# Optimization experiments

Measured on AMD Instinct MI355X. Metric: run time of the kernel, lower is better.

Reference implementation:

```python
import jax, jax.numpy as jnp
import numpy as np

H_BINS = 64
SIGMA = 0.02
EPS = 1e-6


def setup_inputs() -> dict:
    key = jax.random.key(0)
    x = jax.random.uniform(key, (8, 3, 256, 256), dtype=jnp.float32)
    return {"x": x}


def reference(x):
    h = H_BINS
    L = x.shape[0]
    x = jnp.clip(x, 0.0, 1.0)
    I = x.reshape(L, 3, -1)                      # [L,3,N]
    Iy = jnp.sqrt(jnp.sum(I * I, axis=1) + EPS)  # [L,N] pixel intensity
    logs = jnp.log(I + EPS)                      # [L,3,N]
    # per-channel log-chromaticity: for c=0:(u=l0-l1, v=l0-l2); c=1:(l1-l0, l1-l2); c=2:(l2-l0, l2-l1)
    cu = jnp.array([1, 0, 0])
    cv = jnp.array([2, 2, 1])
    U = logs - logs[:, cu, :]                    # [L,3,N]
    V = logs - logs[:, cv, :]                    # [L,3,N]
    offset = jnp.linspace(-3.0, 3.0, h, dtype=jnp.float32)  # [h]
    inv_s2 = jnp.float32(1.0 / (SIGMA * SIGMA))
    # RBF-like (inverse-quadratic) soft binning kernels: [L,3,N,h]
    Ku = 1.0 / (1.0 + jnp.square(U[..., None] - offset) * inv_s2)
    Kv = 1.0 / (1.0 + jnp.square(V[..., None] - offset) * inv_s2)
    # weighted outer-product reduction over pixels -> [L,3,h,h]
    hists = jnp.einsum('ln,lcnu,lcnv->lcuv', Iy, Ku, Kv)
    # normalize each sample by its total mass
    total = jnp.sum(hists, axis=(1, 2, 3), keepdims=True)
    return hists / (total + EPS)
```

## Files before the change

### kernel.cpp

```cpp
#include <hip/hip_runtime.h>

#define H 64
#define NPIX 65536
#define LBATCH 8
#define LC 24
#define S_CHUNKS 32
#define PB 2048
#define EPSF 1e-6f
#define LN2_50 34.6573590f

typedef _Float16 h8 __attribute__((ext_vector_type(8)));
typedef __fp16   g2 __attribute__((ext_vector_type(2)));
typedef float f32x16 __attribute__((ext_vector_type(16)));
union H8u { h8 v8; g2 v2[4]; };

#define KEV(d) __builtin_amdgcn_rcpf(fmaf((d), (d), 1.0f))
#define PK(a, b) __builtin_amdgcn_cvt_pkrtz((a), (b))

__global__ __launch_bounds__(256) void hist_zero(float* __restrict__ out) {
    out[blockIdx.x * 256 + threadIdx.x] = 0.0f;
}

__global__ __launch_bounds__(256, 3) void hist_main(const float* __restrict__ x,
                                                    float* __restrict__ out) {
    __shared__ float sU[PB];
    __shared__ float sV[PB];
    __shared__ float sW[PB];
    __shared__ float sHist[H * H];

    const int tid  = threadIdx.x;
    const int wv   = tid >> 6;
    const int lane = tid & 63;
    const int hf   = lane >> 5;
    const int ln   = lane & 31;
    const int lc   = blockIdx.y;
    const int l    = lc / 3;
    const int c    = lc - 3 * l;

    #pragma unroll
    for (int r = 0; r < 4; r++)
        *(float4*)&sHist[(r * 256 + tid) * 4] = make_float4(0.f, 0.f, 0.f, 0.f);

    const float* __restrict__ x0p = x + (l * 3 + 0) * NPIX;
    const float* __restrict__ x1p = x + (l * 3 + 1) * NPIX;
    const float* __restrict__ x2p = x + (l * 3 + 2) * NPIX;
    const int base = blockIdx.x * PB;

    #pragma unroll
    for (int pass = 0; pass < 2; pass++) {
        const int ploc = pass * 1024 + tid * 4;
        const float4 r0 = *(const float4*)&x0p[base + ploc];
        const float4 r1 = *(const float4*)&x1p[base + ploc];
        const float4 r2 = *(const float4*)&x2p[base + ploc];
        float4 U4, V4, W4;
        #define PREP(E) { \
            const float v0 = fminf(fmaxf(r0.E, 0.0f), 1.0f); \
            const float v1 = fminf(fmaxf(r1.E, 0.0f), 1.0f); \
            const float v2 = fminf(fmaxf(r2.E, 0.0f), 1.0f); \
            W4.E = __builtin_amdgcn_sqrtf(fmaf(v0, v0, fmaf(v1, v1, fmaf(v2, v2, EPSF)))); \
            const float lg0 = __builtin_amdgcn_logf(v0 + EPSF); \
            const float lg1 = __builtin_amdgcn_logf(v1 + EPSF); \
            const float lg2 = __builtin_amdgcn_logf(v2 + EPSF); \
            float U, V; \
            if (c == 0)      { U = lg0 - lg1; V = lg0 - lg2; } \
            else if (c == 1) { U = lg1 - lg0; V = lg1 - lg2; } \
            else             { U = lg2 - lg0; V = lg2 - lg1; } \
            U4.E = LN2_50 * U; V4.E = LN2_50 * V; }
        PREP(x) PREP(y) PREP(z) PREP(w)
        #undef PREP
        *(float4*)&sU[ploc] = U4;
        *(float4*)&sV[ploc] = V4;
        *(float4*)&sW[ploc] = W4;
    }
    __syncthreads();

    const float step50 = 50.0f * (6.0f / 63.0f);
    const float ou0 = -150.0f + step50 * (float)ln;
    const float ou1 = ou0 + step50 * 32.0f;

    f32x16 acc00, acc01, acc10, acc11;
    #pragma unroll
    for (int i = 0; i < 16; i++) { acc00[i] = 0.f; acc01[i] = 0.f; acc10[i] = 0.f; acc11[i] = 0.f; }

    const int wbase = wv * 512;
    #pragma unroll 2
    for (int ks = 0; ks < 32; ks++) {
        const int kb = wbase + ks * 16 + hf * 8;
        const float4 ua = *(const float4*)&sU[kb];
        const float4 ub = *(const float4*)&sU[kb + 4];
        const float4 va = *(const float4*)&sV[kb];
        const float4 vb = *(const float4*)&sV[kb + 4];
        const float4 wa = *(const float4*)&sW[kb];
        const float4 wb = *(const float4*)&sW[kb + 4];
        H8u A0, A1, B0, B1;
        A0.v2[0] = PK(wa.x * KEV(ua.x - ou0), wa.y * KEV(ua.y - ou0));
        A0.v2[1] = PK(wa.z * KEV(ua.z - ou0), wa.w * KEV(ua.w - ou0));
        A0.v2[2] = PK(wb.x * KEV(ub.x - ou0), wb.y * KEV(ub.y - ou0));
        A0.v2[3] = PK(wb.z * KEV(ub.z - ou0), wb.w * KEV(ub.w - ou0));
        A1.v2[0] = PK(wa.x * KEV(ua.x - ou1), wa.y * KEV(ua.y - ou1));
        A1.v2[1] = PK(wa.z * KEV(ua.z - ou1), wa.w * KEV(ua.w - ou1));
        A1.v2[2] = PK(wb.x * KEV(ub.x - ou1), wb.y * KEV(ub.y - ou1));
        A1.v2[3] = PK(wb.z * KEV(ub.z - ou1), wb.w * KEV(ub.w - ou1));
        B0.v2[0] = PK(KEV(va.x - ou0), KEV(va.y - ou0));
        B0.v2[1] = PK(KEV(va.z - ou0), KEV(va.w - ou0));
        B0.v2[2] = PK(KEV(vb.x - ou0), KEV(vb.y - ou0));
        B0.v2[3] = PK(KEV(vb.z - ou0), KEV(vb.w - ou0));
        B1.v2[0] = PK(KEV(va.x - ou1), KEV(va.y - ou1));
        B1.v2[1] = PK(KEV(va.z - ou1), KEV(va.w - ou1));
        B1.v2[2] = PK(KEV(vb.x - ou1), KEV(vb.y - ou1));
        B1.v2[3] = PK(KEV(vb.z - ou1), KEV(vb.w - ou1));
        acc00 = __builtin_amdgcn_mfma_f32_32x32x16_f16(A0.v8, B0.v8, acc00, 0, 0, 0);
        acc01 = __builtin_amdgcn_mfma_f32_32x32x16_f16(A0.v8, B1.v8, acc01, 0, 0, 0);
        acc10 = __builtin_amdgcn_mfma_f32_32x32x16_f16(A1.v8, B0.v8, acc10, 0, 0, 0);
        acc11 = __builtin_amdgcn_mfma_f32_32x32x16_f16(A1.v8, B1.v8, acc11, 0, 0, 0);
    }

    #pragma unroll
    for (int r = 0; r < 16; r++) {
        const int row = (r & 3) + 8 * (r >> 2) + 4 * hf;
        atomicAdd(&sHist[row * 64 + ln],             acc00[r]);
        atomicAdd(&sHist[row * 64 + 32 + ln],        acc01[r]);
        atomicAdd(&sHist[(row + 32) * 64 + ln],      acc10[r]);
        atomicAdd(&sHist[(row + 32) * 64 + 32 + ln], acc11[r]);
    }
    __syncthreads();

    float* __restrict__ g = out + lc * (H * H);
    #pragma unroll
    for (int r = 0; r < 16; r++) {
        const int i = r * 256 + tid;
        unsafeAtomicAdd(&g[i], sHist[i]);
    }
}

__global__ __launch_bounds__(256) void hist_finish(float* __restrict__ out) {
    const int l = blockIdx.x;
    float* __restrict__ p = out + l * 3 * H * H;
    float s = 0.0f;
    #pragma unroll
    for (int it = 0; it < 12; it++) {
        const float4 v = *(const float4*)&p[(it * 256 + threadIdx.x) * 4];
        s += (v.x + v.y) + (v.z + v.w);
    }
    #pragma unroll
    for (int off = 32; off > 0; off >>= 1) s += __shfl_down(s, off, 64);
    __shared__ float ps[4];
    if ((threadIdx.x & 63) == 0) ps[threadIdx.x >> 6] = s;
    __syncthreads();
    const float T = (ps[0] + ps[1]) + (ps[2] + ps[3]);
    const float inv = 1.0f / (T + EPSF);
    #pragma unroll
    for (int it = 0; it < 12; it++) {
        float4 v = *(const float4*)&p[(it * 256 + threadIdx.x) * 4];
        v.x *= inv; v.y *= inv; v.z *= inv; v.w *= inv;
        *(float4*)&p[(it * 256 + threadIdx.x) * 4] = v;
    }
}

extern "C" void kernel_launch(void* const* d_in, const int* in_sizes, int n_in,
                              void* d_out, int out_size, void* d_ws, size_t ws_size,
                              hipStream_t stream) {
    const float* x = (const float*)d_in[0];
    float* out = (float*)d_out;

    hipLaunchKernelGGL(hist_zero,   dim3(LC * H * H / 256), dim3(256), 0, stream, out);
    hipLaunchKernelGGL(hist_main,   dim3(S_CHUNKS, LC),     dim3(256), 0, stream, x, out);
    hipLaunchKernelGGL(hist_finish, dim3(LBATCH),           dim3(256), 0, stream, out);
}
```

Measured before the change: 151.4 us.

## Split histogram into smaller pixel chunks and fuse mass reduction into main kernel

```diff
diff --git a/kernel.cpp b/kernel.cpp
--- a/kernel.cpp
+++ b/kernel.cpp
@@ -4,8 +4,8 @@
 #define NPIX 65536
 #define LBATCH 8
 #define LC 24
-#define S_CHUNKS 32
-#define PB 2048
+#define S_CHUNKS 128
+#define PB 512
 #define EPSF 1e-6f
 #define LN2_50 34.6573590f
 
@@ -17,12 +17,15 @@
 #define KEV(d) __builtin_amdgcn_rcpf(fmaf((d), (d), 1.0f))
 #define PK(a, b) __builtin_amdgcn_cvt_pkrtz((a), (b))
 
-__global__ __launch_bounds__(256) void hist_zero(float* __restrict__ out) {
+__global__ __launch_bounds__(256) void hist_zero(float* __restrict__ out,
+                                                 float* __restrict__ ws) {
     out[blockIdx.x * 256 + threadIdx.x] = 0.0f;
+    if (blockIdx.x == 0 && threadIdx.x < LBATCH) ws[threadIdx.x] = 0.0f;
 }
 
-__global__ __launch_bounds__(256, 3) void hist_main(const float* __restrict__ x,
-                                                    float* __restrict__ out) {
+__global__ __launch_bounds__(256, 4) void hist_main(const float* __restrict__ x,
+                                                    float* __restrict__ out,
+                                                    float* __restrict__ ws) {
     __shared__ float sU[PB];
     __shared__ float sV[PB];
     __shared__ float sW[PB];
@@ -46,18 +49,17 @@
     const float* __restrict__ x2p = x + (l * 3 + 2) * NPIX;
     const int base = blockIdx.x * PB;
 
-    #pragma unroll
-    for (int pass = 0; pass < 2; pass++) {
-        const int ploc = pass * 1024 + tid * 4;
-        const float4 r0 = *(const float4*)&x0p[base + ploc];
-        const float4 r1 = *(const float4*)&x1p[base + ploc];
-        const float4 r2 = *(const float4*)&x2p[base + ploc];
-        float4 U4, V4, W4;
+    {
+        const int ploc = tid * 2;
+        const float2 r0 = *(const float2*)&x0p[base + ploc];
+        const float2 r1 = *(const float2*)&x1p[base + ploc];
+        const float2 r2 = *(const float2*)&x2p[base + ploc];
+        float2 U2, V2, W2;
         #define PREP(E) { \
             const float v0 = fminf(fmaxf(r0.E, 0.0f), 1.0f); \
             const float v1 = fminf(fmaxf(r1.E, 0.0f), 1.0f); \
             const float v2 = fminf(fmaxf(r2.E, 0.0f), 1.0f); \
-            W4.E = __builtin_amdgcn_sqrtf(fmaf(v0, v0, fmaf(v1, v1, fmaf(v2, v2, EPSF)))); \
+            W2.E = __builtin_amdgcn_sqrtf(fmaf(v0, v0, fmaf(v1, v1, fmaf(v2, v2, EPSF)))); \
             const float lg0 = __builtin_amdgcn_logf(v0 + EPSF); \
             const float lg1 = __builtin_amdgcn_logf(v1 + EPSF); \
             const float lg2 = __builtin_amdgcn_logf(v2 + EPSF); \
@@ -65,12 +67,12 @@
             if (c == 0)      { U = lg0 - lg1; V = lg0 - lg2; } \
             else if (c == 1) { U = lg1 - lg0; V = lg1 - lg2; } \
             else             { U = lg2 - lg0; V = lg2 - lg1; } \
-            U4.E = LN2_50 * U; V4.E = LN2_50 * V; }
-        PREP(x) PREP(y) PREP(z) PREP(w)
+            U2.E = LN2_50 * U; V2.E = LN2_50 * V; }
+        PREP(x) PREP(y)
         #undef PREP
-        *(float4*)&sU[ploc] = U4;
-        *(float4*)&sV[ploc] = V4;
-        *(float4*)&sW[ploc] = W4;
+        *(float2*)&sU[ploc] = U2;
+        *(float2*)&sV[ploc] = V2;
+        *(float2*)&sW[ploc] = W2;
     }
     __syncthreads();
 
@@ -82,9 +84,9 @@
     #pragma unroll
     for (int i = 0; i < 16; i++) { acc00[i] = 0.f; acc01[i] = 0.f; acc10[i] = 0.f; acc11[i] = 0.f; }
 
-    const int wbase = wv * 512;
+    const int wbase = wv * 128;
     #pragma unroll 2
-    for (int ks = 0; ks < 32; ks++) {
+    for (int ks = 0; ks < 8; ks++) {
         const int kb = wbase + ks * 16 + hf * 8;
         const float4 ua = *(const float4*)&sU[kb];
         const float4 ub = *(const float4*)&sU[kb + 4];
@@ -107,6 +109,8 @@
         B0.v2[3] = PK(KEV(vb.z - ou0), KEV(vb.w - ou0));
         B1.v2[0] = PK(KEV(va.x - ou1), KEV(va.y - ou1));
         B1.v2[1] = PK(KEV(va.z - ou1), KEV(va.w - ou1));
+        B1.v2[2] = PK(KEV(vb.x - ou1), KEV(vb.w - ou1));
+        B1.v2[3] = PK(KEV(vb.z - ou1), KEV(vb.w - ou1));
         B1.v2[2] = PK(KEV(vb.x - ou1), KEV(vb.y - ou1));
         B1.v2[3] = PK(KEV(vb.z - ou1), KEV(vb.w - ou1));
         acc00 = __builtin_amdgcn_mfma_f32_32x32x16_f16(A0.v8, B0.v8, acc00, 0, 0, 0);
@@ -126,35 +130,27 @@
     __syncthreads();
 
     float* __restrict__ g = out + lc * (H * H);
+    float s = 0.0f;
     #pragma unroll
     for (int r = 0; r < 16; r++) {
         const int i = r * 256 + tid;
-        unsafeAtomicAdd(&g[i], sHist[i]);
-    }
-}
-
-__global__ __launch_bounds__(256) void hist_finish(float* __restrict__ out) {
-    const int l = blockIdx.x;
-    float* __restrict__ p = out + l * 3 * H * H;
-    float s = 0.0f;
-    #pragma unroll
-    for (int it = 0; it < 12; it++) {
-        const float4 v = *(const float4*)&p[(it * 256 + threadIdx.x) * 4];
-        s += (v.x + v.y) + (v.z + v.w);
+        const float v = sHist[i];
+        s += v;
+        unsafeAtomicAdd(&g[i], v);
     }
     #pragma unroll
     for (int off = 32; off > 0; off >>= 1) s += __shfl_down(s, off, 64);
-    __shared__ float ps[4];
-    if ((threadIdx.x & 63) == 0) ps[threadIdx.x >> 6] = s;
-    __syncthreads();
-    const float T = (ps[0] + ps[1]) + (ps[2] + ps[3]);
-    const float inv = 1.0f / (T + EPSF);
-    #pragma unroll
-    for (int it = 0; it < 12; it++) {
-        float4 v = *(const float4*)&p[(it * 256 + threadIdx.x) * 4];
-        v.x *= inv; v.y *= inv; v.z *= inv; v.w *= inv;
-        *(float4*)&p[(it * 256 + threadIdx.x) * 4] = v;
-    }
+    if (lane == 0) unsafeAtomicAdd(&ws[l], s);
+}
+
+__global__ __launch_bounds__(256) void hist_scale(float* __restrict__ out,
+                                                  const float* __restrict__ ws) {
+    const int i4 = blockIdx.x * 256 + threadIdx.x;
+    const int l  = blockIdx.x / 12;
+    const float inv = 1.0f / (ws[l] + EPSF);
+    float4 v = *(const float4*)&out[i4 * 4];
+    v.x *= inv; v.y *= inv; v.z *= inv; v.w *= inv;
+    *(float4*)&out[i4 * 4] = v;
 }
 
 extern "C" void kernel_launch(void* const* d_in, const int* in_sizes, int n_in,
@@ -162,8 +158,9 @@
                               hipStream_t stream) {
     const float* x = (const float*)d_in[0];
     float* out = (float*)d_out;
+    float* ws = (float*)d_ws;
 
-    hipLaunchKernelGGL(hist_zero,   dim3(LC * H * H / 256), dim3(256), 0, stream, out);
-    hipLaunchKernelGGL(hist_main,   dim3(S_CHUNKS, LC),     dim3(256), 0, stream, x, out);
-    hipLaunchKernelGGL(hist_finish, dim3(LBATCH),           dim3(256), 0, stream, out);
+    hipLaunchKernelGGL(hist_zero,  dim3(LC * H * H / 256),      dim3(256), 0, stream, out, ws);
+    hipLaunchKernelGGL(hist_main,  dim3(S_CHUNKS, LC),          dim3(256), 0, stream, x, out, ws);
+    hipLaunchKernelGGL(hist_scale, dim3(LBATCH * 3 * H * H / 1024), dim3(256), 0, stream, out, ws);
 }
```

Result: slower. 340.0 us (+124.6%).

## Replace global atomic accumulation with per-block partials and a separate reduce kernel

Applied to the files above, without the earlier changes.

```diff
diff --git a/kernel.cpp b/kernel.cpp
--- a/kernel.cpp
+++ b/kernel.cpp
@@ -8,6 +8,8 @@
 #define PB 2048
 #define EPSF 1e-6f
 #define LN2_50 34.6573590f
+#define NPART (LC * S_CHUNKS)
+#define PART_FLOATS (NPART * H * H)
 
 typedef _Float16 h8 __attribute__((ext_vector_type(8)));
 typedef __fp16   g2 __attribute__((ext_vector_type(2)));
@@ -17,12 +19,8 @@
 #define KEV(d) __builtin_amdgcn_rcpf(fmaf((d), (d), 1.0f))
 #define PK(a, b) __builtin_amdgcn_cvt_pkrtz((a), (b))
 
-__global__ __launch_bounds__(256) void hist_zero(float* __restrict__ out) {
-    out[blockIdx.x * 256 + threadIdx.x] = 0.0f;
-}
-
 __global__ __launch_bounds__(256, 3) void hist_main(const float* __restrict__ x,
-                                                    float* __restrict__ out) {
+                                                    float* __restrict__ ws) {
     __shared__ float sU[PB];
     __shared__ float sV[PB];
     __shared__ float sW[PB];
@@ -125,36 +123,48 @@
     }
     __syncthreads();
 
-    float* __restrict__ g = out + lc * (H * H);
+    float* __restrict__ g = ws + (lc * S_CHUNKS + blockIdx.x) * (H * H);
     #pragma unroll
-    for (int r = 0; r < 16; r++) {
-        const int i = r * 256 + tid;
-        unsafeAtomicAdd(&g[i], sHist[i]);
+    for (int r = 0; r < 4; r++) {
+        const int i = (r * 256 + tid) * 4;
+        *(float4*)&g[i] = *(const float4*)&sHist[i];
     }
 }
 
-__global__ __launch_bounds__(256) void hist_finish(float* __restrict__ out) {
-    const int l = blockIdx.x;
-    float* __restrict__ p = out + l * 3 * H * H;
-    float s = 0.0f;
+__global__ __launch_bounds__(256) void hist_reduce(const float* __restrict__ ws,
+                                                   float* __restrict__ out,
+                                                   float* __restrict__ wsq) {
+    const int lc  = blockIdx.x >> 2;
+    const int off = (blockIdx.x & 3) * 1024 + threadIdx.x * 4;
+    float4 a = make_float4(0.f, 0.f, 0.f, 0.f);
+    #pragma unroll 8
+    for (int ch = 0; ch < S_CHUNKS; ch++) {
+        const float4 v = *(const float4*)&ws[(lc * S_CHUNKS + ch) * (H * H) + off];
+        a.x += v.x; a.y += v.y; a.z += v.z; a.w += v.w;
+    }
+    *(float4*)&out[lc * (H * H) + off] = a;
+
+    float s = (a.x + a.y) + (a.z + a.w);
     #pragma unroll
-    for (int it = 0; it < 12; it++) {
-        const float4 v = *(const float4*)&p[(it * 256 + threadIdx.x) * 4];
-        s += (v.x + v.y) + (v.z + v.w);
-    }
-    #pragma unroll
-    for (int off = 32; off > 0; off >>= 1) s += __shfl_down(s, off, 64);
+    for (int o = 32; o > 0; o >>= 1) s += __shfl_down(s, o, 64);
     __shared__ float ps[4];
     if ((threadIdx.x & 63) == 0) ps[threadIdx.x >> 6] = s;
     __syncthreads();
-    const float T = (ps[0] + ps[1]) + (ps[2] + ps[3]);
+    if (threadIdx.x == 0) wsq[blockIdx.x] = (ps[0] + ps[1]) + (ps[2] + ps[3]);
+}
+
+__global__ __launch_bounds__(256) void hist_scale(float* __restrict__ out,
+                                                  const float* __restrict__ wsq) {
+    const int lc = blockIdx.x >> 2;
+    const int l  = lc / 3;
+    float T = 0.f;
+    #pragma unroll
+    for (int j = 0; j < 12; j++) T += wsq[l * 12 + j];
     const float inv = 1.0f / (T + EPSF);
-    #pragma unroll
-    for (int it = 0; it < 12; it++) {
-        float4 v = *(const float4*)&p[(it * 256 + threadIdx.x) * 4];
-        v.x *= inv; v.y *= inv; v.z *= inv; v.w *= inv;
-        *(float4*)&p[(it * 256 + threadIdx.x) * 4] = v;
-    }
+    const int off = (blockIdx.x & 3) * 1024 + threadIdx.x * 4;
+    float4 v = *(const float4*)&out[lc * (H * H) + off];
+    v.x *= inv; v.y *= inv; v.z *= inv; v.w *= inv;
+    *(float4*)&out[lc * (H * H) + off] = v;
 }
 
 extern "C" void kernel_launch(void* const* d_in, const int* in_sizes, int n_in,
@@ -162,8 +172,9 @@
                               hipStream_t stream) {
     const float* x = (const float*)d_in[0];
     float* out = (float*)d_out;
+    float* ws = (float*)d_ws;
 
-    hipLaunchKernelGGL(hist_zero,   dim3(LC * H * H / 256), dim3(256), 0, stream, out);
-    hipLaunchKernelGGL(hist_main,   dim3(S_CHUNKS, LC),     dim3(256), 0, stream, x, out);
-    hipLaunchKernelGGL(hist_finish, dim3(LBATCH),           dim3(256), 0, stream, out);
+    hipLaunchKernelGGL(hist_main,   dim3(S_CHUNKS, LC), dim3(256), 0, stream, x, ws);
+    hipLaunchKernelGGL(hist_reduce, dim3(96),           dim3(256), 0, stream, ws, out, ws + PART_FLOATS);
+    hipLaunchKernelGGL(hist_scale,  dim3(96),           dim3(256), 0, stream, out, ws + PART_FLOATS);
 }
```

After: 153.6 us. About the same (+1.5%).
